# Performance work log

Measured on AMD Instinct MI355X. Metric: run time of the kernel, lower is better.

## Reference

```python
import jax, jax.numpy as jnp
import numpy as np

B, N, DIN, DOUT, L = 32, 512, 768, 256, 512
NEG = -9.0e15
SLOPE = 0.2  # LeakyReLU negative slope


def setup_inputs() -> dict:
    key = jax.random.key(0)
    ks = jax.random.split(key, 7)
    h = jax.random.normal(ks[0], (B, N, DIN), dtype=jnp.float32)
    adj = jax.random.randint(ks[1], (B, N, N), 0, 2, dtype=jnp.int32)
    positions = jax.random.randint(ks[2], (B, N), 0, L, dtype=jnp.int32)
    W = jax.random.normal(ks[3], (DIN, DOUT), dtype=jnp.float32) * 0.02
    a1 = jax.random.normal(ks[4], (DOUT,), dtype=jnp.float32) * 0.02
    a2 = jax.random.normal(ks[5], (DOUT,), dtype=jnp.float32) * 0.02
    pos_table = jax.random.normal(ks[6], (L, DOUT), dtype=jnp.float32) * 0.02
    return {"h": h, "adj": adj, "positions": positions, "W": W,
            "a1": a1, "a2": a2, "pos_table": pos_table}


def reference(h, adj, positions, W, a1, a2, pos_table):
    # Wh = W(h) + pos_emb(positions)   -> [B, N, DOUT]
    Wh = jnp.einsum('bnd,de->bne', h, W) + pos_table[positions]
    # Pairwise GAT score: e_ij = leakyrelu(a1 . Wh_i + a2 . Wh_j)
    # (identical math to concat([Wh_i, Wh_j]) @ [a1; a2], without the O(N^2*2D) tensor)
    s1 = jnp.einsum('bnd,d->bn', Wh, a1)  # source term   [B, N]
    s2 = jnp.einsum('bnd,d->bn', Wh, a2)  # target term   [B, N]
    e = jax.nn.leaky_relu(s1[:, :, None] + s2[:, None, :], negative_slope=SLOPE)  # [B,N,N]
    # adjacency mask + softmax over neighbors (dropout is identity in eval)
    attention = jax.nn.softmax(jnp.where(adj > 0, e, NEG), axis=-1)  # [B, N, N]
    h_prime = jnp.einsum('bij,bjd->bid', attention, Wh)  # [B, N, DOUT]
    return h_prime, attention
```

## Files before the change

### kernel.cpp

```cpp
#include <hip/hip_runtime.h>
#include <math.h>

#define B 32
#define N 512
#define DIN 768
#define DOUT 256
#define NEGV -9.0e15f
#define SLOPE 0.2f

typedef __bf16 bf16x8 __attribute__((ext_vector_type(8)));
typedef float f32x4 __attribute__((ext_vector_type(4)));
typedef unsigned short us8 __attribute__((ext_vector_type(8)));

__device__ __forceinline__ unsigned short f2b(float f) {
    union { float f; unsigned u; } v; v.f = f;
    unsigned r = v.u + 0x7FFF + ((v.u >> 16) & 1);
    return (unsigned short)(r >> 16);
}

__device__ __forceinline__ void gload_lds16(const unsigned short* g, unsigned short* l) {
    __builtin_amdgcn_global_load_lds(
        (const __attribute__((address_space(1))) unsigned int*)(unsigned long long)(uintptr_t)g,
        (__attribute__((address_space(3))) unsigned int*)(uintptr_t)l,
        16, 0, 0);
}

__global__ __launch_bounds__(256) void conv_fused(
    const float4* __restrict__ hin, ushort4* __restrict__ hout,
    const float* __restrict__ W, unsigned short* __restrict__ WT) {
    __shared__ unsigned short tile[64][65];
    const int t = threadIdx.x;
    if (blockIdx.x < 12288) {
        int idx = blockIdx.x * 256 + t;
        float4 v = hin[idx];
        ushort4 o;
        o.x = f2b(v.x); o.y = f2b(v.y); o.z = f2b(v.z); o.w = f2b(v.w);
        hout[idx] = o;
    } else {
        int bid = blockIdx.x - 12288;
        int k0 = (bid % 12) * 64, n0 = (bid / 12) * 64;
        const int cl = t & 63, cg = t >> 6;
#pragma unroll
        for (int i = 0; i < 16; ++i) {
            int k = cg * 16 + i;
            tile[cl][k] = f2b(W[(size_t)(k0 + k) * DOUT + n0 + cl]);
        }
        __syncthreads();
#pragma unroll
        for (int i = 0; i < 16; ++i) {
            int n = cg * 16 + i;
            WT[(size_t)(n0 + n) * DIN + k0 + cl] = tile[n][cl];
        }
    }
}

__global__ __launch_bounds__(256) void wh_mfma(
    const unsigned short* __restrict__ hA,
    const unsigned short* __restrict__ WT,
    const int*   __restrict__ pos,
    const float* __restrict__ ptab,
    const float* __restrict__ a1,
    const float* __restrict__ a2,
    unsigned short* __restrict__ WhT,
    float* __restrict__ s1, float* __restrict__ s2)
{
    constexpr int K = DIN;
    __shared__ unsigned short smem[12288];
    unsigned short* As = smem;
    unsigned short* Bs = smem + 8192;
    unsigned short* tileT = smem;

    const int t    = threadIdx.x;
    const int lane = t & 63;
    const int w    = t >> 6;
    const int lin  = blockIdx.x;
    const int m0   = (lin & 127) * 128;
    const int n0   = (lin >> 7) * 64;

    int arow[4], apos[4];
#pragma unroll
    for (int i = 0; i < 4; ++i) {
        int c = i * 256 + t;
        arow[i] = c >> 3;
        apos[i] = (c & 7) ^ ((c >> 3) & 7);
    }
    int brow[2], bpos[2];
#pragma unroll
    for (int i = 0; i < 2; ++i) {
        int c = i * 256 + t;
        brow[i] = c >> 3;
        bpos[i] = (c & 7) ^ ((c >> 3) & 7);
    }
    const unsigned short* gA[4];
    const unsigned short* gB[2];
#pragma unroll
    for (int i = 0; i < 4; ++i) gA[i] = hA + (size_t)(m0 + arow[i]) * K + apos[i] * 8;
#pragma unroll
    for (int i = 0; i < 2; ++i) gB[i] = WT + (size_t)(n0 + brow[i]) * K + bpos[i] * 8;
    unsigned short* lA[4];
    unsigned short* lB[2];
#pragma unroll
    for (int i = 0; i < 4; ++i) lA[i] = As + (i * 256 + (t & 192)) * 8;
#pragma unroll
    for (int i = 0; i < 2; ++i) lB[i] = Bs + (i * 256 + (t & 192)) * 8;

    const int wm = (w & 1) * 64, wn = (w >> 1) * 32;
    const int l15 = lane & 15, q = lane >> 4;
    int aoff[2][4], boff[2][2];
#pragma unroll
    for (int kk = 0; kk < 2; ++kk) {
        int pg = kk * 4 + q;
#pragma unroll
        for (int i = 0; i < 4; ++i) {
            int rm = wm + i * 16 + l15;
            aoff[kk][i] = rm * 64 + ((pg ^ (rm & 7)) * 8);
        }
#pragma unroll
        for (int i = 0; i < 2; ++i) {
            int rn = wn + i * 16 + l15;
            boff[kk][i] = rn * 64 + ((pg ^ (rn & 7)) * 8);
        }
    }

    f32x4 acc[4][2];
#pragma unroll
    for (int i = 0; i < 4; ++i)
#pragma unroll
        for (int j = 0; j < 2; ++j) acc[i][j] = (f32x4){0.f, 0.f, 0.f, 0.f};

    for (int k0 = 0; k0 < K; k0 += 64) {
#pragma unroll
        for (int i = 0; i < 4; ++i) gload_lds16(gA[i] + k0, lA[i]);
#pragma unroll
        for (int i = 0; i < 2; ++i) gload_lds16(gB[i] + k0, lB[i]);
        __syncthreads();
#pragma unroll
        for (int kk = 0; kk < 2; ++kk) {
            bf16x8 af[4], bfr[2];
#pragma unroll
            for (int i = 0; i < 4; ++i) af[i] = *(const bf16x8*)(As + aoff[kk][i]);
#pragma unroll
            for (int i = 0; i < 2; ++i) bfr[i] = *(const bf16x8*)(Bs + boff[kk][i]);
#pragma unroll
            for (int mi = 0; mi < 4; ++mi)
#pragma unroll
                for (int ni = 0; ni < 2; ++ni)
                    acc[mi][ni] = __builtin_amdgcn_mfma_f32_16x16x32_bf16(
                        af[mi], bfr[ni], acc[mi][ni], 0, 0, 0);
        }
        __syncthreads();
    }

    const float a1v[2] = { a1[n0 + wn + l15], a1[n0 + wn + 16 + l15] };
    const float a2v[2] = { a2[n0 + wn + l15], a2[n0 + wn + 16 + l15] };
#pragma unroll
    for (int mi = 0; mi < 4; ++mi) {
        const int jb = wm + mi * 16 + q * 4;
        float v[2][4];
#pragma unroll
        for (int ni = 0; ni < 2; ++ni) {
            const int nl = wn + ni * 16 + l15;
            ushort4 pk;
            unsigned short* pp = (unsigned short*)&pk;
#pragma unroll
            for (int r = 0; r < 4; ++r) {
                int m = m0 + jb + r;
                int p = pos[m];
                float val = acc[mi][ni][r] + ptab[(size_t)p * DOUT + n0 + nl];
                v[ni][r] = val;
                pp[r] = f2b(val);
            }
            *(ushort4*)&tileT[nl * 136 + jb] = pk;
        }
#pragma unroll
        for (int r = 0; r < 4; ++r) {
            float t1 = v[0][r] * a1v[0] + v[1][r] * a1v[1];
            float t2 = v[0][r] * a2v[0] + v[1][r] * a2v[1];
#pragma unroll
            for (int mk = 1; mk < 16; mk <<= 1) {
                t1 += __shfl_xor(t1, mk);
                t2 += __shfl_xor(t2, mk);
            }
            if (l15 == 0) {
                atomicAdd(&s1[m0 + jb + r], t1);
                atomicAdd(&s2[m0 + jb + r], t2);
            }
        }
    }
    __syncthreads();
    const int bb = m0 >> 9, j0 = m0 & 511;
#pragma unroll
    for (int rr = 0; rr < 4; ++rr) {
        int nl = (t >> 4) + rr * 16;
        int jl = (t & 15) * 8;
        us8 vv = *(const us8*)&tileT[nl * 136 + jl];
        *(us8*)&WhT[((size_t)bb * DOUT + n0 + nl) * N + j0 + jl] = vv;
    }
}

__global__ __launch_bounds__(512) void attn_hp(
    const float* __restrict__ s1,
    const float* __restrict__ s2,
    const int*   __restrict__ adj,
    const unsigned short* __restrict__ WhT,
    float* __restrict__ att,
    float* __restrict__ hp)
{
    __shared__ unsigned short P[64 * 512];

    const int t    = threadIdx.x;
    const int lane = t & 63;
    const int w    = t >> 6;
    const int bb   = blockIdx.x >> 3;
    const int m0   = (blockIdx.x & 7) * 64;

    {
        const int r = t >> 3, c = t & 7;
        const size_t rowg = (size_t)bb * N + m0 + r;
        const float s1i = s1[rowg];
        const int4*   adjp = (const int4*)(adj + rowg * N + c * 64);
        const float4* s2p  = (const float4*)(s2 + (size_t)bb * N + c * 64);
        float fe[64];
        float mx = -3.0e38f;
#pragma unroll
        for (int i = 0; i < 16; ++i) {
            int4 a = adjp[i];
            float4 sv = s2p[i];
            float v0 = s1i + sv.x; v0 = v0 > 0.f ? v0 : SLOPE * v0; v0 = (a.x > 0) ? v0 : NEGV;
            float v1 = s1i + sv.y; v1 = v1 > 0.f ? v1 : SLOPE * v1; v1 = (a.y > 0) ? v1 : NEGV;
            float v2 = s1i + sv.z; v2 = v2 > 0.f ? v2 : SLOPE * v2; v2 = (a.z > 0) ? v2 : NEGV;
            float v3 = s1i + sv.w; v3 = v3 > 0.f ? v3 : SLOPE * v3; v3 = (a.w > 0) ? v3 : NEGV;
            fe[i * 4 + 0] = v0; fe[i * 4 + 1] = v1;
            fe[i * 4 + 2] = v2; fe[i * 4 + 3] = v3;
            mx = fmaxf(mx, fmaxf(fmaxf(v0, v1), fmaxf(v2, v3)));
        }
#pragma unroll
        for (int mk = 1; mk < 8; mk <<= 1) mx = fmaxf(mx, __shfl_xor(mx, mk));
        float sum = 0.f;
#pragma unroll
        for (int k = 0; k < 64; ++k) { fe[k] = __expf(fe[k] - mx); sum += fe[k]; }
#pragma unroll
        for (int mk = 1; mk < 8; mk <<= 1) sum += __shfl_xor(sum, mk);
        const float inv = 1.0f / sum;

        float* attrow = att + rowg * N + c * 64;
#pragma unroll
        for (int i = 0; i < 16; ++i) {
            float4 o = { fe[i * 4 + 0] * inv, fe[i * 4 + 1] * inv,
                         fe[i * 4 + 2] * inv, fe[i * 4 + 3] * inv };
            ((float4*)attrow)[i] = o;
        }
#pragma unroll
        for (int jj = 0; jj < 8; ++jj) {
            int slot = c * 8 + jj;
            int S = slot ^ (r & 7) ^ c;
            bf16x8 pv;
#pragma unroll
            for (int e = 0; e < 8; ++e) pv[e] = (__bf16)(fe[jj * 8 + e] * inv);
            *(bf16x8*)&P[r * 512 + S * 8] = pv;
        }
    }
    __syncthreads();

    const int wn  = w * 32;
    const int l15 = lane & 15, q = lane >> 4;
    const unsigned short* bRow[2];
#pragma unroll
    for (int ni = 0; ni < 2; ++ni)
        bRow[ni] = WhT + ((size_t)bb * DOUT + wn + ni * 16 + l15) * N + q * 8;
    int rm7[4], rmBase[4];
#pragma unroll
    for (int mi = 0; mi < 4; ++mi) {
        int rm = mi * 16 + l15;
        rm7[mi] = rm & 7;
        rmBase[mi] = rm * 512;
    }

    f32x4 acc[4][2];
#pragma unroll
    for (int i = 0; i < 4; ++i)
#pragma unroll
        for (int j = 0; j < 2; ++j) acc[i][j] = (f32x4){0.f, 0.f, 0.f, 0.f};

#pragma unroll 4
    for (int k0 = 0; k0 < N; k0 += 32) {
        const int slot = (k0 >> 3) + q;
        const int hi = slot >> 3;
        bf16x8 af[4], bfr[2];
#pragma unroll
        for (int ni = 0; ni < 2; ++ni)
            bfr[ni] = *(const bf16x8*)(bRow[ni] + k0);
#pragma unroll
        for (int mi = 0; mi < 4; ++mi) {
            int S = slot ^ rm7[mi] ^ hi;
            af[mi] = *(const bf16x8*)&P[rmBase[mi] + S * 8];
        }
#pragma unroll
        for (int mi = 0; mi < 4; ++mi)
#pragma unroll
            for (int ni = 0; ni < 2; ++ni)
                acc[mi][ni] = __builtin_amdgcn_mfma_f32_16x16x32_bf16(
                    af[mi], bfr[ni], acc[mi][ni], 0, 0, 0);
    }

#pragma unroll
    for (int mi = 0; mi < 4; ++mi) {
#pragma unroll
        for (int rr = 0; rr < 4; ++rr) {
            int m = m0 + mi * 16 + q * 4 + rr;
#pragma unroll
            for (int ni = 0; ni < 2; ++ni) {
                int n = wn + ni * 16 + l15;
                hp[((size_t)bb * N + m) * DOUT + n] = acc[mi][ni][rr];
            }
        }
    }
}

extern "C" void kernel_launch(void* const* d_in, const int* in_sizes, int n_in,
                              void* d_out, int out_size, void* d_ws, size_t ws_size,
                              hipStream_t stream) {
    const float* h         = (const float*)d_in[0];
    const int*   adj       = (const int*)  d_in[1];
    const int*   positions = (const int*)  d_in[2];
    const float* W         = (const float*)d_in[3];
    const float* a1        = (const float*)d_in[4];
    const float* a2        = (const float*)d_in[5];
    const float* pos_table = (const float*)d_in[6];

    float* out     = (float*)d_out;
    float* h_prime = out;
    float* att     = out + (size_t)B * N * DOUT;

    char* ws = (char*)d_ws;
    unsigned short* h_bf = (unsigned short*)ws;
    unsigned short* WT   = (unsigned short*)(ws + 25165824);
    unsigned short* WhT  = (unsigned short*)(ws + 25559040);
    float*          s1   = (float*)(ws + 33947648);
    float*          s2   = s1 + (size_t)B * N;

    hipMemsetAsync(s1, 0, (size_t)2 * B * N * sizeof(float), stream);
    conv_fused<<<12288 + 48, 256, 0, stream>>>((const float4*)h, (ushort4*)h_bf, W, WT);
    wh_mfma<<<512, 256, 0, stream>>>(h_bf, WT, positions, pos_table, a1, a2, WhT, s1, s2);
    attn_hp<<<256, 512, 0, stream>>>(s1, s2, adj, WhT, att, h_prime);
}
```

Baseline: 173.0 us.

## Recompute softmax scores from bitmask instead of holding 64 floats in registers

The softmax prologue no longer keeps a 64-float score array per thread. It packs the adjacency predicate into a 64-bit mask and recomputes the LeakyReLU scores in three passes (max, sum, write), re-reading s2 each time. The column assignment is also interleaved so the 8 threads of a row read adjacent float4s, which coalesces the adj, s2 and att accesses. The bf16 P tile is written as ushort4 with an adjusted XOR swizzle. This lowers register pressure and improves memory coalescing, at the cost of extra exp evaluations and repeated s2 loads.

New measurement: 171.2 us. About the same (-1.0%).

```diff
diff --git a/kernel.cpp b/kernel.cpp
--- a/kernel.cpp
+++ b/kernel.cpp
@@ -218,46 +218,73 @@
         const int r = t >> 3, c = t & 7;
         const size_t rowg = (size_t)bb * N + m0 + r;
         const float s1i = s1[rowg];
-        const int4*   adjp = (const int4*)(adj + rowg * N + c * 64);
-        const float4* s2p  = (const float4*)(s2 + (size_t)bb * N + c * 64);
-        float fe[64];
+        const int4*   adjp = (const int4*)(adj + rowg * N) + c;
+        const float4* s2p  = (const float4*)(s2 + (size_t)bb * N) + c;
+
+        unsigned long long msk = 0ull;
         float mx = -3.0e38f;
-#pragma unroll
-        for (int i = 0; i < 16; ++i) {
-            int4 a = adjp[i];
-            float4 sv = s2p[i];
-            float v0 = s1i + sv.x; v0 = v0 > 0.f ? v0 : SLOPE * v0; v0 = (a.x > 0) ? v0 : NEGV;
-            float v1 = s1i + sv.y; v1 = v1 > 0.f ? v1 : SLOPE * v1; v1 = (a.y > 0) ? v1 : NEGV;
-            float v2 = s1i + sv.z; v2 = v2 > 0.f ? v2 : SLOPE * v2; v2 = (a.z > 0) ? v2 : NEGV;
-            float v3 = s1i + sv.w; v3 = v3 > 0.f ? v3 : SLOPE * v3; v3 = (a.w > 0) ? v3 : NEGV;
-            fe[i * 4 + 0] = v0; fe[i * 4 + 1] = v1;
-            fe[i * 4 + 2] = v2; fe[i * 4 + 3] = v3;
+#pragma unroll 4
+        for (int i = 0; i < 16; ++i) {
+            int4 a = adjp[i * 8];
+            float4 sv = s2p[i * 8];
+            float v0 = s1i + sv.x; v0 = v0 > 0.f ? v0 : SLOPE * v0;
+            float v1 = s1i + sv.y; v1 = v1 > 0.f ? v1 : SLOPE * v1;
+            float v2 = s1i + sv.z; v2 = v2 > 0.f ? v2 : SLOPE * v2;
+            float v3 = s1i + sv.w; v3 = v3 > 0.f ? v3 : SLOPE * v3;
+            v0 = (a.x > 0) ? v0 : NEGV;
+            v1 = (a.y > 0) ? v1 : NEGV;
+            v2 = (a.z > 0) ? v2 : NEGV;
+            v3 = (a.w > 0) ? v3 : NEGV;
+            unsigned bits = (a.x > 0 ? 1u : 0u) | (a.y > 0 ? 2u : 0u) |
+                            (a.z > 0 ? 4u : 0u) | (a.w > 0 ? 8u : 0u);
+            msk |= (unsigned long long)bits << (i * 4);
             mx = fmaxf(mx, fmaxf(fmaxf(v0, v1), fmaxf(v2, v3)));
         }
 #pragma unroll
         for (int mk = 1; mk < 8; mk <<= 1) mx = fmaxf(mx, __shfl_xor(mx, mk));
+
         float sum = 0.f;
-#pragma unroll
-        for (int k = 0; k < 64; ++k) { fe[k] = __expf(fe[k] - mx); sum += fe[k]; }
+#pragma unroll 4
+        for (int i = 0; i < 16; ++i) {
+            float4 sv = s2p[i * 8];
+            float v0 = s1i + sv.x; v0 = v0 > 0.f ? v0 : SLOPE * v0;
+            float v1 = s1i + sv.y; v1 = v1 > 0.f ? v1 : SLOPE * v1;
+            float v2 = s1i + sv.z; v2 = v2 > 0.f ? v2 : SLOPE * v2;
+            float v3 = s1i + sv.w; v3 = v3 > 0.f ? v3 : SLOPE * v3;
+            v0 = ((msk >> (i * 4 + 0)) & 1) ? v0 : NEGV;
+            v1 = ((msk >> (i * 4 + 1)) & 1) ? v1 : NEGV;
+            v2 = ((msk >> (i * 4 + 2)) & 1) ? v2 : NEGV;
+            v3 = ((msk >> (i * 4 + 3)) & 1) ? v3 : NEGV;
+            sum += __expf(v0 - mx) + __expf(v1 - mx) +
+                   __expf(v2 - mx) + __expf(v3 - mx);
+        }
 #pragma unroll
         for (int mk = 1; mk < 8; mk <<= 1) sum += __shfl_xor(sum, mk);
         const float inv = 1.0f / sum;
 
-        float* attrow = att + rowg * N + c * 64;
-#pragma unroll
-        for (int i = 0; i < 16; ++i) {
-            float4 o = { fe[i * 4 + 0] * inv, fe[i * 4 + 1] * inv,
-                         fe[i * 4 + 2] * inv, fe[i * 4 + 3] * inv };
-            ((float4*)attrow)[i] = o;
-        }
-#pragma unroll
-        for (int jj = 0; jj < 8; ++jj) {
-            int slot = c * 8 + jj;
-            int S = slot ^ (r & 7) ^ c;
-            bf16x8 pv;
-#pragma unroll
-            for (int e = 0; e < 8; ++e) pv[e] = (__bf16)(fe[jj * 8 + e] * inv);
-            *(bf16x8*)&P[r * 512 + S * 8] = pv;
+        float4* attrow = (float4*)(att + rowg * N);
+        unsigned short* Prow = P + r * 512;
+        const int r7 = r & 7, chalf = (c & 1) * 4;
+#pragma unroll 4
+        for (int i = 0; i < 16; ++i) {
+            float4 sv = s2p[i * 8];
+            float v0 = s1i + sv.x; v0 = v0 > 0.f ? v0 : SLOPE * v0;
+            float v1 = s1i + sv.y; v1 = v1 > 0.f ? v1 : SLOPE * v1;
+            float v2 = s1i + sv.z; v2 = v2 > 0.f ? v2 : SLOPE * v2;
+            float v3 = s1i + sv.w; v3 = v3 > 0.f ? v3 : SLOPE * v3;
+            v0 = ((msk >> (i * 4 + 0)) & 1) ? v0 : NEGV;
+            v1 = ((msk >> (i * 4 + 1)) & 1) ? v1 : NEGV;
+            v2 = ((msk >> (i * 4 + 2)) & 1) ? v2 : NEGV;
+            v3 = ((msk >> (i * 4 + 3)) & 1) ? v3 : NEGV;
+            float e0 = __expf(v0 - mx) * inv;
+            float e1 = __expf(v1 - mx) * inv;
+            float e2 = __expf(v2 - mx) * inv;
+            float e3 = __expf(v3 - mx) * inv;
+            attrow[i * 8 + c] = (float4){e0, e1, e2, e3};
+            int slot = i * 4 + (c >> 1);
+            int S = slot ^ r7 ^ (slot >> 3);
+            ushort4 pk = { f2b(e0), f2b(e1), f2b(e2), f2b(e3) };
+            *(ushort4*)&Prow[S * 8 + chalf] = pk;
         }
     }
     __syncthreads();
```
